# Kernel optimization log

Measured on AMD Instinct MI355X. Metric: run time of the kernel, lower is better.

## Reference

```python
import jax, jax.numpy as jnp
import numpy as np

B, L, D_IN = 2, 4096, 512
H, D_K, D_V, D_OUT = 8, 64, 64, 512


def setup_inputs() -> dict:
    key = jax.random.key(0)
    k0, k1, k2, k3, k4 = jax.random.split(key, 5)
    x = jax.random.normal(k0, (B, L, D_IN), dtype=jnp.float32)
    W_q = jax.random.uniform(k1, (H, D_IN, D_K), dtype=jnp.float32)
    W_k = jax.random.uniform(k2, (H, D_IN, D_K), dtype=jnp.float32)
    W_v = jax.random.uniform(k3, (H, D_IN, D_V), dtype=jnp.float32)
    W_o = jax.random.uniform(k4, (H, D_V, D_OUT), dtype=jnp.float32)
    return {"x": x, "W_q": W_q, "W_k": W_k, "W_v": W_v, "W_o": W_o}


def reference(x, W_q, W_k, W_v, W_o):
    # x: (b, l, d_in); projections per head -> (b, h, l, d)
    Q = jnp.einsum('hjk,blj->bhlk', W_q, x)
    K = jnp.einsum('hjk,blj->bhlk', W_k, x)
    V = jnp.einsum('hjv,blj->bhlv', W_v, x)
    # no softmax: pure bilinear attention (Q K^T) V
    scores = jnp.einsum('bhik,bhjk->bhij', Q, K)          # (b, h, l, l)
    values = jnp.einsum('bhqk,bhkv->bhqv', scores, V)     # (b, h, l, d_v)
    return jnp.einsum('hvo,bhlv->blo', W_o, values)       # (b, l, d_out)
```

## Files before the change

kernel.cpp:

```cpp
#include <hip/hip_runtime.h>
#include <cstdint>


#define BDIM 2
#define LDIM 4096
#define DIN 512
#define HDIM 8
#define DK 64
#define DV 64
#define DOUT 512
#define NS 8

using bf16_t = __bf16;
typedef __bf16 bf16x8 __attribute__((ext_vector_type(8)));
typedef float floatx4 __attribute__((ext_vector_type(4)));

__device__ __forceinline__ unsigned short f2bf(float f) {
    unsigned int u = __builtin_bit_cast(unsigned int, f);
    u += 0x7FFFu + ((u >> 16) & 1u);
    return (unsigned short)(u >> 16);
}

__device__ __forceinline__ void gld_lds16(const void* g, void* l) {
    __builtin_amdgcn_global_load_lds(
        (const __attribute__((address_space(1))) void*)g,
        (__attribute__((address_space(3))) void*)l, 16, 0, 0);
}

template <int BM, int BN, int BK, bool TRANS_OUT, int OUT_MODE>
__device__ __forceinline__ void gemm_core(const bf16_t* A, const bf16_t* B,
                                          void* Cp, int K, int lda, int ldb,
                                          int ldc, int tm, int tn) {
    constexpr int WM = BM / 2, WN = BN / 2;
    constexpr int FM = WM / 16, FN = WN / 16;
    constexpr int CPR = BK / 8;
    __shared__ bf16_t As[BM * BK];
    __shared__ bf16_t Bs[BN * BK];
    const int tid = threadIdx.x;
    const int lane = tid & 63;
    const int wr = (tid >> 7) & 1;
    const int wc = (tid >> 6) & 1;

    A += (size_t)tm * lda;
    B += (size_t)tn * ldb;

    floatx4 acc[FM][FN] = {};

    for (int k0 = 0; k0 < K; k0 += BK) {
#pragma unroll
        for (int i = 0; i < (BM * CPR) / 256; ++i) {
            int c = i * 256 + tid;
            int m = c / CPR, kc = c % CPR;
            gld_lds16(A + (size_t)m * lda + k0 + kc * 8, As + c * 8);
        }
#pragma unroll
        for (int i = 0; i < (BN * CPR) / 256; ++i) {
            int c = i * 256 + tid;
            int m = c / CPR, kc = c % CPR;
            gld_lds16(B + (size_t)m * ldb + k0 + kc * 8, Bs + c * 8);
        }
        __syncthreads();

#pragma unroll
        for (int kk = 0; kk < BK; kk += 32) {
            bf16x8 aF[FM], bF[FN];
#pragma unroll
            for (int fm = 0; fm < FM; ++fm)
                aF[fm] = *(const bf16x8*)(As + (wr * WM + fm * 16 + (lane & 15)) * BK +
                                          kk + (lane >> 4) * 8);
#pragma unroll
            for (int fn = 0; fn < FN; ++fn)
                bF[fn] = *(const bf16x8*)(Bs + (wc * WN + fn * 16 + (lane & 15)) * BK +
                                          kk + (lane >> 4) * 8);
#pragma unroll
            for (int fm = 0; fm < FM; ++fm)
#pragma unroll
                for (int fn = 0; fn < FN; ++fn)
                    acc[fm][fn] = __builtin_amdgcn_mfma_f32_16x16x32_bf16(
                        aF[fm], bF[fn], acc[fm][fn], 0, 0, 0);
        }
        __syncthreads();
    }

    const int cr4 = (lane >> 4) * 4;
    const int cn = lane & 15;
#pragma unroll
    for (int fm = 0; fm < FM; ++fm)
#pragma unroll
        for (int fn = 0; fn < FN; ++fn)
#pragma unroll
            for (int r = 0; r < 4; ++r) {
                int m = tm + wr * WM + fm * 16 + cr4 + r;
                int n = tn + wc * WN + fn * 16 + cn;
                size_t idx = TRANS_OUT ? ((size_t)n * ldc + m)
                                       : ((size_t)m * ldc + n);
                if (OUT_MODE == 0)
                    ((float*)Cp)[idx] = acc[fm][fn][r];
                else
                    ((unsigned short*)Cp)[idx] = f2bf(acc[fm][fn][r]);
            }
}

__global__ __launch_bounds__(256) void k_gram(const bf16_t* xT, float* Gp) {
    int z = blockIdx.z, b = z / NS, s = z % NS;
    const bf16_t* Ab = xT + (size_t)b * DIN * LDIM + s * (LDIM / NS);
    gemm_core<128, 128, 64, false, 0>(Ab, Ab, Gp + (size_t)z * DIN * DIN,
                                      LDIM / NS, LDIM, LDIM, DIN,
                                      blockIdx.x * 128, blockIdx.y * 128);
}

__global__ __launch_bounds__(256) void k_gred(const float* Gp, unsigned short* G16) {
    size_t idx = ((size_t)blockIdx.x * 256 + threadIdx.x) * 4;
    int b = (int)(idx >> 18);
    size_t r = idx & (((size_t)1 << 18) - 1);
    float4 s = make_float4(0.f, 0.f, 0.f, 0.f);
#pragma unroll
    for (int sl = 0; sl < NS; ++sl) {
        float4 v = *(const float4*)(Gp + (((size_t)(b * NS + sl)) << 18) + r);
        s.x += v.x; s.y += v.y; s.z += v.z; s.w += v.w;
    }
    *(ushort4*)(G16 + idx) =
        make_ushort4(f2bf(s.x), f2bf(s.y), f2bf(s.z), f2bf(s.w));
}

__global__ __launch_bounds__(256) void k_proj(const bf16_t* G16, const bf16_t* WvT,
                                              unsigned short* UT) {
    int b = blockIdx.z;
    gemm_core<64, 64, 32, true, 1>(G16 + (size_t)b * DIN * DIN, WvT,
                                   UT + (size_t)b * DIN * DIN, DIN, DIN, DIN,
                                   DIN, blockIdx.x * 64, blockIdx.y * 64);
}

__global__ __launch_bounds__(256) void k_kvnw(const bf16_t* WkT, const bf16_t* UT,
                                              const bf16_t* WoT, unsigned short* NT) {
    int mo = blockIdx.x;
    int b = blockIdx.y >> 3, h = blockIdx.y & 7;
    __shared__ bf16_t As[64 * 32];
    __shared__ bf16_t Bs[64 * 32];
    __shared__ bf16_t Ms[64 * 64];
    __shared__ bf16_t Aw[64 * 64];
    const int tid = threadIdx.x;
    const int lane = tid & 63;
    const int wr = (tid >> 7) & 1, wc = (tid >> 6) & 1;
    const int cr4 = (lane >> 4) * 4, cn = lane & 15;

    const bf16_t* A = WkT + (size_t)h * DK * DIN;
    const bf16_t* B = UT + (size_t)b * DIN * DIN + (size_t)h * DV * DIN;
    floatx4 acc[2][2] = {};
    for (int k0 = 0; k0 < DIN; k0 += 32) {
        int c = tid, m = c >> 2, kc = c & 3;
        gld_lds16(A + (size_t)m * DIN + k0 + kc * 8, As + c * 8);
        gld_lds16(B + (size_t)m * DIN + k0 + kc * 8, Bs + c * 8);
        __syncthreads();
        bf16x8 aF[2], bF[2];
#pragma unroll
        for (int f = 0; f < 2; ++f) {
            aF[f] = *(const bf16x8*)(As + (wr * 32 + f * 16 + cn) * 32 + (lane >> 4) * 8);
            bF[f] = *(const bf16x8*)(Bs + (wc * 32 + f * 16 + cn) * 32 + (lane >> 4) * 8);
        }
#pragma unroll
        for (int fm = 0; fm < 2; ++fm)
#pragma unroll
            for (int fn = 0; fn < 2; ++fn)
                acc[fm][fn] = __builtin_amdgcn_mfma_f32_16x16x32_bf16(
                    aF[fm], bF[fn], acc[fm][fn], 0, 0, 0);
        __syncthreads();
    }
#pragma unroll
    for (int fm = 0; fm < 2; ++fm)
#pragma unroll
        for (int fn = 0; fn < 2; ++fn)
#pragma unroll
            for (int r = 0; r < 4; ++r) {
                int m = wr * 32 + fm * 16 + cr4 + r;
                int n = wc * 32 + fn * 16 + cn;
                ((unsigned short*)Ms)[m * 64 + n] = f2bf(acc[fm][fn][r]);
            }

    const bf16_t* Ao = WoT + (size_t)h * DOUT * DV;
    unsigned short* NTb = NT + (size_t)b * DOUT * DIN + h * DK;
#pragma unroll
    for (int i = 0; i < 2; ++i) {
        int c = i * 256 + tid, m = c >> 3, kc = c & 7;
        gld_lds16(Ao + (size_t)(mo * 64 + m) * DV + kc * 8, Aw + c * 8);
    }
    __syncthreads();
    floatx4 a2[2][2] = {};
#pragma unroll
    for (int k0 = 0; k0 < 64; k0 += 32) {
        bf16x8 aF[2], bF[2];
#pragma unroll
        for (int f = 0; f < 2; ++f) {
            aF[f] = *(const bf16x8*)(Aw + (wr * 32 + f * 16 + cn) * 64 + k0 + (lane >> 4) * 8);
            bF[f] = *(const bf16x8*)(Ms + (wc * 32 + f * 16 + cn) * 64 + k0 + (lane >> 4) * 8);
        }
#pragma unroll
        for (int fm = 0; fm < 2; ++fm)
#pragma unroll
            for (int fn = 0; fn < 2; ++fn)
                a2[fm][fn] = __builtin_amdgcn_mfma_f32_16x16x32_bf16(
                    aF[fm], bF[fn], a2[fm][fn], 0, 0, 0);
    }
#pragma unroll
    for (int fm = 0; fm < 2; ++fm)
#pragma unroll
        for (int fn = 0; fn < 2; ++fn)
#pragma unroll
            for (int r = 0; r < 4; ++r) {
                int m = wr * 32 + fm * 16 + cr4 + r;
                int n = wc * 32 + fn * 16 + cn;
                NTb[(size_t)(mo * 64 + m) * DIN + n] = f2bf(a2[fm][fn][r]);
            }
}

__global__ __launch_bounds__(256) void k_cw(const bf16_t* Wq_cat, const bf16_t* NT,
                                            unsigned short* CT) {
    int b = blockIdx.z;
    gemm_core<64, 64, 32, true, 1>(Wq_cat, NT + (size_t)b * DOUT * DIN,
                                   CT + (size_t)b * DIN * DOUT, DIN, DIN, DIN,
                                   DIN, blockIdx.x * 64, blockIdx.y * 64);
}

__global__ __launch_bounds__(256) void k_out(const bf16_t* x16, const bf16_t* CT,
                                             float* out) {
    int b = blockIdx.z;
    gemm_core<128, 128, 64, false, 0>(x16 + (size_t)b * LDIM * DIN,
                                      CT + (size_t)b * DIN * DOUT,
                                      out + (size_t)b * LDIM * DOUT, DIN, DIN,
                                      DIN, DOUT, blockIdx.x * 128,
                                      blockIdx.y * 128);
}

__global__ __launch_bounds__(256) void k_prep2(
    const float* x, const float* Wq, const float* Wk, const float* Wv,
    const float* Wo, unsigned short* xb, unsigned short* xT,
    unsigned short* WqC, unsigned short* WkT, unsigned short* WvT,
    unsigned short* WoT) {
    __shared__ unsigned short T[64][65];
    int tr = threadIdx.x >> 4, tc4 = (threadIdx.x & 15) * 4;
    int bid = blockIdx.x;
    if (bid < 1024) {
        int b = bid >> 9, r = bid & 511;
        int d0 = (r & 7) * 64, l0 = (r >> 3) * 64;
        const float* xp = x + (size_t)b * LDIM * DIN;
        unsigned short* xbp = xb + (size_t)b * LDIM * DIN;
#pragma unroll
        for (int p = 0; p < 4; ++p) {
            int l = p * 16 + tr;
            float4 v = *(const float4*)(xp + (size_t)(l0 + l) * DIN + d0 + tc4);
            unsigned short q0 = f2bf(v.x), q1 = f2bf(v.y), q2 = f2bf(v.z),
                           q3 = f2bf(v.w);
            *(ushort4*)(xbp + (size_t)(l0 + l) * DIN + d0 + tc4) =
                make_ushort4(q0, q1, q2, q3);
            T[l][tc4 + 0] = q0; T[l][tc4 + 1] = q1;
            T[l][tc4 + 2] = q2; T[l][tc4 + 3] = q3;
        }
        __syncthreads();
        unsigned short* xTp = xT + (size_t)b * DIN * LDIM;
#pragma unroll
        for (int p = 0; p < 4; ++p) {
            int d = p * 16 + tr;
            ushort4 u = make_ushort4(T[tc4 + 0][d], T[tc4 + 1][d], T[tc4 + 2][d],
                                     T[tc4 + 3][d]);
            *(ushort4*)(xTp + (size_t)(d0 + d) * LDIM + l0 + tc4) = u;
        }
        return;
    }
    int p_ = bid - 1024;
    int t = p_ & 7, job = (p_ >> 3) & 3, h = p_ >> 5;
    if (job == 0) {
        const float* src = Wq + (size_t)h * DIN * DK;
#pragma unroll
        for (int p = 0; p < 4; ++p) {
            int i = t * 64 + p * 16 + tr;
            float4 v = *(const float4*)(src + (size_t)i * DK + tc4);
            *(ushort4*)(WqC + (size_t)i * (HDIM * DK) + h * DK + tc4) =
                make_ushort4(f2bf(v.x), f2bf(v.y), f2bf(v.z), f2bf(v.w));
        }
        return;
    }
    const float* src;
    unsigned short* dst;
    int rows, cols, r0, c0;
    if (job == 1) {
        src = Wk + (size_t)h * DIN * DK; dst = WkT + (size_t)h * DK * DIN;
        rows = DIN; cols = DK; r0 = t * 64; c0 = 0;
    } else if (job == 2) {
        src = Wv + (size_t)h * DIN * DV; dst = WvT + (size_t)h * DV * DIN;
        rows = DIN; cols = DV; r0 = t * 64; c0 = 0;
    } else {
        src = Wo + (size_t)h * DV * DOUT; dst = WoT + (size_t)h * DOUT * DV;
        rows = DV; cols = DOUT; r0 = 0; c0 = t * 64;
    }
#pragma unroll
    for (int p = 0; p < 4; ++p) {
        int r = p * 16 + tr;
        float4 v = *(const float4*)(src + (size_t)(r0 + r) * cols + c0 + tc4);
        T[r][tc4 + 0] = f2bf(v.x); T[r][tc4 + 1] = f2bf(v.y);
        T[r][tc4 + 2] = f2bf(v.z); T[r][tc4 + 3] = f2bf(v.w);
    }
    __syncthreads();
#pragma unroll
    for (int p = 0; p < 4; ++p) {
        int c = p * 16 + tr;
        ushort4 u = make_ushort4(T[tc4 + 0][c], T[tc4 + 1][c], T[tc4 + 2][c],
                                 T[tc4 + 3][c]);
        *(ushort4*)(dst + (size_t)(c0 + c) * rows + r0 + tc4) = u;
    }
}

extern "C" void kernel_launch(void* const* d_in, const int* in_sizes, int n_in,
                              void* d_out, int out_size, void* d_ws, size_t ws_size,
                              hipStream_t stream) {
    const float* x  = (const float*)d_in[0];
    const float* Wq = (const float*)d_in[1];
    const float* Wk = (const float*)d_in[2];
    const float* Wv = (const float*)d_in[3];
    const float* Wo = (const float*)d_in[4];
    float* out = (float*)d_out;

    unsigned short* w = (unsigned short*)d_ws;
    unsigned short* xb16  = w; w += (size_t)BDIM * LDIM * DIN;
    unsigned short* xT16  = w; w += (size_t)BDIM * DIN * LDIM;
    unsigned short* WqC   = w; w += (size_t)DIN * HDIM * DK;
    unsigned short* WkT   = w; w += (size_t)HDIM * DK * DIN;
    unsigned short* WvT   = w; w += (size_t)HDIM * DV * DIN;
    unsigned short* WoT   = w; w += (size_t)HDIM * DOUT * DV;
    unsigned short* G16   = w; w += (size_t)BDIM * DIN * DIN;
    unsigned short* UT    = w; w += (size_t)BDIM * DIN * DIN;
    unsigned short* NT    = w; w += (size_t)BDIM * DOUT * DIN;
    unsigned short* CT    = w; w += (size_t)BDIM * DIN * DOUT;
    float* Gp = (float*)(((uintptr_t)w + 255) & ~(uintptr_t)255);

    k_prep2<<<dim3(1280), 256, 0, stream>>>(x, Wq, Wk, Wv, Wo, xb16, xT16,
                                            WqC, WkT, WvT, WoT);
    k_gram<<<dim3(4, 4, BDIM * NS), 256, 0, stream>>>((const bf16_t*)xT16, Gp);
    k_gred<<<dim3((BDIM * DIN * DIN) / 1024), 256, 0, stream>>>(Gp, G16);
    k_proj<<<dim3(8, 8, BDIM), 256, 0, stream>>>((const bf16_t*)G16,
                                                 (const bf16_t*)WvT, UT);
    k_kvnw<<<dim3(8, BDIM * HDIM), 256, 0, stream>>>((const bf16_t*)WkT,
                                                     (const bf16_t*)UT,
                                                     (const bf16_t*)WoT, NT);
    k_cw<<<dim3(8, 8, BDIM), 256, 0, stream>>>((const bf16_t*)WqC,
                                               (const bf16_t*)NT, CT);
    k_out<<<dim3(LDIM / 128, DOUT / 128, BDIM), 256, 0, stream>>>(
        (const bf16_t*)xb16, (const bf16_t*)CT, out);
}
```

Baseline: 133.5 us.

## Split Gram over more slices, store partials in bf16, restructure tail kernels

Doubles the number of L-slices in the Gram computation for more parallelism and stores the partial Gram matrices as bf16 instead of fp32, halving partial-sum traffic in the reduction. The reduction kernel now sums eight bf16 values per thread. The kvnw/cw pair is replaced by a small per-head M kernel plus a fused tail kernel that builds C directly, looping over heads and skipping the NT intermediate. The output GEMM tile is shrunk to 64x128 to launch more blocks. Rounding partials to bf16 adds precision loss, and the k_m launch runs only 16 blocks.

```diff
diff --git a/kernel.cpp b/kernel.cpp
--- a/kernel.cpp
+++ b/kernel.cpp
@@ -9,7 +9,7 @@
 #define DK 64
 #define DV 64
 #define DOUT 512
-#define NS 8
+#define NS 16
 
 using bf16_t = __bf16;
 typedef __bf16 bf16x8 __attribute__((ext_vector_type(8)));
@@ -19,6 +19,11 @@
     unsigned int u = __builtin_bit_cast(unsigned int, f);
     u += 0x7FFFu + ((u >> 16) & 1u);
     return (unsigned short)(u >> 16);
+}
+
+__device__ __forceinline__ float bf2f(unsigned short s) {
+    unsigned int u = ((unsigned int)s) << 16;
+    return __builtin_bit_cast(float, u);
 }
 
 __device__ __forceinline__ void gld_lds16(const void* g, void* l) {
@@ -101,26 +106,35 @@
             }
 }
 
-__global__ __launch_bounds__(256) void k_gram(const bf16_t* xT, float* Gp) {
+__global__ __launch_bounds__(256) void k_gram(const bf16_t* xT, unsigned short* Gp) {
     int z = blockIdx.z, b = z / NS, s = z % NS;
     const bf16_t* Ab = xT + (size_t)b * DIN * LDIM + s * (LDIM / NS);
-    gemm_core<128, 128, 64, false, 0>(Ab, Ab, Gp + (size_t)z * DIN * DIN,
+    gemm_core<128, 128, 64, false, 1>(Ab, Ab, Gp + (size_t)z * DIN * DIN,
                                       LDIM / NS, LDIM, LDIM, DIN,
                                       blockIdx.x * 128, blockIdx.y * 128);
 }
 
-__global__ __launch_bounds__(256) void k_gred(const float* Gp, unsigned short* G16) {
-    size_t idx = ((size_t)blockIdx.x * 256 + threadIdx.x) * 4;
-    int b = (int)(idx >> 18);
-    size_t r = idx & (((size_t)1 << 18) - 1);
-    float4 s = make_float4(0.f, 0.f, 0.f, 0.f);
+__global__ __launch_bounds__(256) void k_gred(const unsigned short* Gp,
+                                              unsigned short* G16) {
+    size_t gid = (size_t)blockIdx.x * 256 + threadIdx.x;
+    int b = (int)(gid >> 15);
+    size_t r = (gid & 32767) * 8;
+    float s[8] = {};
 #pragma unroll
     for (int sl = 0; sl < NS; ++sl) {
-        float4 v = *(const float4*)(Gp + (((size_t)(b * NS + sl)) << 18) + r);
-        s.x += v.x; s.y += v.y; s.z += v.z; s.w += v.w;
-    }
-    *(ushort4*)(G16 + idx) =
-        make_ushort4(f2bf(s.x), f2bf(s.y), f2bf(s.z), f2bf(s.w));
+        const unsigned short* p = Gp + (((size_t)(b * NS + sl)) << 18) + r;
+        uint4 v = *(const uint4*)p;
+        unsigned int ws[4] = {v.x, v.y, v.z, v.w};
+#pragma unroll
+        for (int q = 0; q < 4; ++q) {
+            s[q * 2 + 0] += bf2f((unsigned short)(ws[q] & 0xffffu));
+            s[q * 2 + 1] += bf2f((unsigned short)(ws[q] >> 16));
+        }
+    }
+    unsigned short o[8];
+#pragma unroll
+    for (int q = 0; q < 8; ++q) o[q] = f2bf(s[q]);
+    *(uint4*)(G16 + (((size_t)b) << 18) + r) = *(const uint4*)o;
 }
 
 __global__ __launch_bounds__(256) void k_proj(const bf16_t* G16, const bf16_t* WvT,
@@ -131,41 +145,91 @@
                                    DIN, blockIdx.x * 64, blockIdx.y * 64);
 }
 
-__global__ __launch_bounds__(256) void k_kvnw(const bf16_t* WkT, const bf16_t* UT,
-                                              const bf16_t* WoT, unsigned short* NT) {
-    int mo = blockIdx.x;
-    int b = blockIdx.y >> 3, h = blockIdx.y & 7;
-    __shared__ bf16_t As[64 * 32];
-    __shared__ bf16_t Bs[64 * 32];
-    __shared__ bf16_t Ms[64 * 64];
-    __shared__ bf16_t Aw[64 * 64];
+__global__ __launch_bounds__(256) void k_m(const bf16_t* WkT, const bf16_t* UT,
+                                           unsigned short* M) {
+    int z = blockIdx.x, b = z >> 3, h = z & 7;
+    gemm_core<64, 64, 32, false, 1>(WkT + (size_t)h * DK * DIN,
+                                    UT + (size_t)b * DIN * DIN + (size_t)h * DV * DIN,
+                                    M + (size_t)z * DK * DV, DIN, DIN, DIN, DV,
+                                    0, 0);
+}
+
+__global__ __launch_bounds__(256) void k_tail(const bf16_t* WqC, const bf16_t* WoT,
+                                              const bf16_t* M, unsigned short* CT) {
+    int i0 = blockIdx.x * 64, o0 = blockIdx.y * 64, b = blockIdx.z;
+    __shared__ bf16_t Aq[64 * 64];
+    __shared__ bf16_t Ws[64 * 64];
+    __shared__ bf16_t Msh[64 * 64];
+    __shared__ bf16_t PTs[64 * 64];
     const int tid = threadIdx.x;
     const int lane = tid & 63;
     const int wr = (tid >> 7) & 1, wc = (tid >> 6) & 1;
     const int cr4 = (lane >> 4) * 4, cn = lane & 15;
 
-    const bf16_t* A = WkT + (size_t)h * DK * DIN;
-    const bf16_t* B = UT + (size_t)b * DIN * DIN + (size_t)h * DV * DIN;
     floatx4 acc[2][2] = {};
-    for (int k0 = 0; k0 < DIN; k0 += 32) {
-        int c = tid, m = c >> 2, kc = c & 3;
-        gld_lds16(A + (size_t)m * DIN + k0 + kc * 8, As + c * 8);
-        gld_lds16(B + (size_t)m * DIN + k0 + kc * 8, Bs + c * 8);
-        __syncthreads();
-        bf16x8 aF[2], bF[2];
-#pragma unroll
-        for (int f = 0; f < 2; ++f) {
-            aF[f] = *(const bf16x8*)(As + (wr * 32 + f * 16 + cn) * 32 + (lane >> 4) * 8);
-            bF[f] = *(const bf16x8*)(Bs + (wc * 32 + f * 16 + cn) * 32 + (lane >> 4) * 8);
+
+    for (int h = 0; h < HDIM; ++h) {
+#pragma unroll
+        for (int i = 0; i < 2; ++i) {
+            int c = i * 256 + tid, m = c >> 3, kc = c & 7;
+            gld_lds16(WqC + (size_t)(i0 + m) * DIN + h * 64 + kc * 8, Aq + c * 8);
+            gld_lds16(WoT + ((size_t)h * DOUT + o0 + m) * DV + kc * 8, Ws + c * 8);
+            gld_lds16(M + (((size_t)(b * HDIM + h)) << 12) + m * 64 + kc * 8,
+                      Msh + c * 8);
+        }
+        __syncthreads();
+
+        floatx4 pt[2][2] = {};
+#pragma unroll
+        for (int kk = 0; kk < 64; kk += 32) {
+            bf16x8 aF[2], bF[2];
+#pragma unroll
+            for (int f = 0; f < 2; ++f) {
+                aF[f] = *(const bf16x8*)(Ws + (wr * 32 + f * 16 + cn) * 64 + kk +
+                                         (lane >> 4) * 8);
+                bF[f] = *(const bf16x8*)(Msh + (wc * 32 + f * 16 + cn) * 64 + kk +
+                                         (lane >> 4) * 8);
+            }
+#pragma unroll
+            for (int fm = 0; fm < 2; ++fm)
+#pragma unroll
+                for (int fn = 0; fn < 2; ++fn)
+                    pt[fm][fn] = __builtin_amdgcn_mfma_f32_16x16x32_bf16(
+                        aF[fm], bF[fn], pt[fm][fn], 0, 0, 0);
         }
 #pragma unroll
         for (int fm = 0; fm < 2; ++fm)
 #pragma unroll
             for (int fn = 0; fn < 2; ++fn)
-                acc[fm][fn] = __builtin_amdgcn_mfma_f32_16x16x32_bf16(
-                    aF[fm], bF[fn], acc[fm][fn], 0, 0, 0);
-        __syncthreads();
-    }
+#pragma unroll
+                for (int r = 0; r < 4; ++r) {
+                    int m = wr * 32 + fm * 16 + cr4 + r;
+                    int n = wc * 32 + fn * 16 + cn;
+                    ((unsigned short*)PTs)[m * 64 + n] = f2bf(pt[fm][fn][r]);
+                }
+        __syncthreads();
+
+#pragma unroll
+        for (int kk = 0; kk < 64; kk += 32) {
+            bf16x8 aF[2], bF[2];
+#pragma unroll
+            for (int f = 0; f < 2; ++f) {
+                aF[f] = *(const bf16x8*)(PTs + (wr * 32 + f * 16 + cn) * 64 + kk +
+                                         (lane >> 4) * 8);
+                bF[f] = *(const bf16x8*)(Aq + (wc * 32 + f * 16 + cn) * 64 + kk +
+                                         (lane >> 4) * 8);
+            }
+#pragma unroll
+            for (int fm = 0; fm < 2; ++fm)
+#pragma unroll
+                for (int fn = 0; fn < 2; ++fn)
+                    acc[fm][fn] = __builtin_amdgcn_mfma_f32_16x16x32_bf16(
+                        aF[fm], bF[fn], acc[fm][fn], 0, 0, 0);
+        }
+        __syncthreads();
+    }
+
+    unsigned short* CTb = CT + (size_t)b * DIN * DOUT;
 #pragma unroll
     for (int fm = 0; fm < 2; ++fm)
 #pragma unroll
@@ -174,61 +238,18 @@
             for (int r = 0; r < 4; ++r) {
                 int m = wr * 32 + fm * 16 + cr4 + r;
                 int n = wc * 32 + fn * 16 + cn;
-                ((unsigned short*)Ms)[m * 64 + n] = f2bf(acc[fm][fn][r]);
+                CTb[(size_t)(o0 + m) * DIN + i0 + n] = f2bf(acc[fm][fn][r]);
             }
-
-    const bf16_t* Ao = WoT + (size_t)h * DOUT * DV;
-    unsigned short* NTb = NT + (size_t)b * DOUT * DIN + h * DK;
-#pragma unroll
-    for (int i = 0; i < 2; ++i) {
-        int c = i * 256 + tid, m = c >> 3, kc = c & 7;
-        gld_lds16(Ao + (size_t)(mo * 64 + m) * DV + kc * 8, Aw + c * 8);
-    }
-    __syncthreads();
-    floatx4 a2[2][2] = {};
-#pragma unroll
-    for (int k0 = 0; k0 < 64; k0 += 32) {
-        bf16x8 aF[2], bF[2];
-#pragma unroll
-        for (int f = 0; f < 2; ++f) {
-            aF[f] = *(const bf16x8*)(Aw + (wr * 32 + f * 16 + cn) * 64 + k0 + (lane >> 4) * 8);
-            bF[f] = *(const bf16x8*)(Ms + (wc * 32 + f * 16 + cn) * 64 + k0 + (lane >> 4) * 8);
-        }
-#pragma unroll
-        for (int fm = 0; fm < 2; ++fm)
-#pragma unroll
-            for (int fn = 0; fn < 2; ++fn)
-                a2[fm][fn] = __builtin_amdgcn_mfma_f32_16x16x32_bf16(
-                    aF[fm], bF[fn], a2[fm][fn], 0, 0, 0);
-    }
-#pragma unroll
-    for (int fm = 0; fm < 2; ++fm)
-#pragma unroll
-        for (int fn = 0; fn < 2; ++fn)
-#pragma unroll
-            for (int r = 0; r < 4; ++r) {
-                int m = wr * 32 + fm * 16 + cr4 + r;
-                int n = wc * 32 + fn * 16 + cn;
-                NTb[(size_t)(mo * 64 + m) * DIN + n] = f2bf(a2[fm][fn][r]);
-            }
-}
-
-__global__ __launch_bounds__(256) void k_cw(const bf16_t* Wq_cat, const bf16_t* NT,
-                                            unsigned short* CT) {
-    int b = blockIdx.z;
-    gemm_core<64, 64, 32, true, 1>(Wq_cat, NT + (size_t)b * DOUT * DIN,
-                                   CT + (size_t)b * DIN * DOUT, DIN, DIN, DIN,
-                                   DIN, blockIdx.x * 64, blockIdx.y * 64);
 }
 
 __global__ __launch_bounds__(256) void k_out(const bf16_t* x16, const bf16_t* CT,
                                              float* out) {
     int b = blockIdx.z;
-    gemm_core<128, 128, 64, false, 0>(x16 + (size_t)b * LDIM * DIN,
-                                      CT + (size_t)b * DIN * DOUT,
-                                      out + (size_t)b * LDIM * DOUT, DIN, DIN,
-                                      DIN, DOUT, blockIdx.x * 128,
-                                      blockIdx.y * 128);
+    gemm_core<64, 128, 64, false, 0>(x16 + (size_t)b * LDIM * DIN,
+                                     CT + (size_t)b * DIN * DOUT,
+                                     out + (size_t)b * LDIM * DOUT, DIN, DIN,
+                                     DIN, DOUT, blockIdx.x * 64,
+                                     blockIdx.y * 128);
 }
 
 __global__ __launch_bounds__(256) void k_prep2(
@@ -328,21 +349,21 @@
     unsigned short* WoT   = w; w += (size_t)HDIM * DOUT * DV;
     unsigned short* G16   = w; w += (size_t)BDIM * DIN * DIN;
     unsigned short* UT    = w; w += (size_t)BDIM * DIN * DIN;
-    unsigned short* NT    = w; w += (size_t)BDIM * DOUT * DIN;
+    unsigned short* Mbuf  = w; w += (size_t)BDIM * HDIM * DK * DV;
     unsigned short* CT    = w; w += (size_t)BDIM * DIN * DOUT;
-    float* Gp = (float*)(((uintptr_t)w + 255) & ~(uintptr_t)255);
+    unsigned short* Gp    = w; w += (size_t)BDIM * NS * DIN * DIN;
 
     k_prep2<<<dim3(1280), 256, 0, stream>>>(x, Wq, Wk, Wv, Wo, xb16, xT16,
                                             WqC, WkT, WvT, WoT);
     k_gram<<<dim3(4, 4, BDIM * NS), 256, 0, stream>>>((const bf16_t*)xT16, Gp);
-    k_gred<<<dim3((BDIM * DIN * DIN) / 1024), 256, 0, stream>>>(Gp, G16);
+    k_gred<<<dim3((BDIM * DIN * DIN) / (256 * 8)), 256, 0, stream>>>(Gp, G16);
     k_proj<<<dim3(8, 8, BDIM), 256, 0, stream>>>((const bf16_t*)G16,
                                                  (const bf16_t*)WvT, UT);
-    k_kvnw<<<dim3(8, BDIM * HDIM), 256, 0, stream>>>((const bf16_t*)WkT,
-                                                     (const bf16_t*)UT,
-                                                     (const bf16_t*)WoT, NT);
-    k_cw<<<dim3(8, 8, BDIM), 256, 0, stream>>>((const bf16_t*)WqC,
-                                               (const bf16_t*)NT, CT);
-    k_out<<<dim3(LDIM / 128, DOUT / 128, BDIM), 256, 0, stream>>>(
+    k_m<<<dim3(BDIM * HDIM), 256, 0, stream>>>((const bf16_t*)WkT,
+                                               (const bf16_t*)UT, Mbuf);
+    k_tail<<<dim3(8, 8, BDIM), 256, 0, stream>>>((const bf16_t*)WqC,
+                                                 (const bf16_t*)WoT,
+                                                 (const bf16_t*)Mbuf, CT);
+    k_out<<<dim3(LDIM / 64, DOUT / 128, BDIM), 256, 0, stream>>>(
         (const bf16_t*)xb16, (const bf16_t*)CT, out);
 }
```

Result: no change. 131.5 us (-1.4%).
